# Kernel tuning notes

Hardware: AMD Instinct MI355X
Metric: run time of the kernel (lower is better)

## Reference

```python
import jax, jax.numpy as jnp
import numpy as np

POS_SCALE = 50.0
LEN_SCALE = 500.0

N_NODES = 100000
N_EDGES = 600000
IN_DIM = 128
HID_DIM = 128


def setup_inputs() -> dict:
    key = jax.random.key(0)
    ks = jax.random.split(key, 12)
    x = jax.random.normal(ks[0], (N_NODES, IN_DIM), dtype=jnp.float32)
    positions = jax.random.randint(ks[1], (N_NODES,), 0, 50, dtype=jnp.int64)
    lengths = jax.random.randint(ks[2], (N_NODES,), 0, 500, dtype=jnp.int64)
    edge_index = jax.random.randint(ks[3], (2, N_EDGES), 0, N_NODES, dtype=jnp.int64)
    reranker_scores = jax.random.normal(ks[4], (N_NODES,), dtype=jnp.float32)
    s = 1.0 / np.sqrt(IN_DIM + 2)
    fp_w = jax.random.uniform(ks[5], (IN_DIM + 2, IN_DIM), minval=-s, maxval=s, dtype=jnp.float32)
    fp_b = jnp.zeros((IN_DIM,), jnp.float32)
    s2 = 1.0 / np.sqrt(IN_DIM)
    lin_l_w = jax.random.uniform(ks[6], (IN_DIM, HID_DIM), minval=-s2, maxval=s2, dtype=jnp.float32)
    lin_l_b = jnp.zeros((HID_DIM,), jnp.float32)
    lin_r_w = jax.random.uniform(ks[7], (IN_DIM, HID_DIM), minval=-s2, maxval=s2, dtype=jnp.float32)
    res_w = jax.random.uniform(ks[8], (IN_DIM, HID_DIM), minval=-s2, maxval=s2, dtype=jnp.float32)
    res_b = jnp.zeros((HID_DIM,), jnp.float32)
    s3 = 1.0 / np.sqrt(HID_DIM)
    sh_w = jax.random.uniform(ks[9], (HID_DIM, 1), minval=-s3, maxval=s3, dtype=jnp.float32)
    sh_b = jnp.zeros((1,), jnp.float32)
    alpha = jnp.asarray(0.65, jnp.float32)
    return {
        "x": x, "positions": positions, "lengths": lengths,
        "edge_index": edge_index, "reranker_scores": reranker_scores,
        "fp_w": fp_w, "fp_b": fp_b,
        "lin_l_w": lin_l_w, "lin_l_b": lin_l_b, "lin_r_w": lin_r_w,
        "res_w": res_w, "res_b": res_b,
        "sh_w": sh_w, "sh_b": sh_b, "alpha": alpha,
    }


def reference(x, positions, lengths, edge_index, reranker_scores,
              fp_w, fp_b, lin_l_w, lin_l_b, lin_r_w, res_w, res_b,
              sh_w, sh_b, alpha):
    n = x.shape[0]
    # position/length features
    pos_feat = positions[:, None].astype(x.dtype) / POS_SCALE
    len_feat = lengths[:, None].astype(x.dtype) / LEN_SCALE
    xf = jnp.concatenate([x, pos_feat, len_feat], axis=-1)  # [N, D+2]
    xf = xf @ fp_w + fp_b                                   # [N, D]
    h_in = xf @ res_w + res_b                               # residual proj [N, H]
    # SAGEConv with mean aggregation: out = lin_l(mean_{j->i} x_j) + lin_r(x_i)
    src, dst = edge_index[0], edge_index[1]
    msg_sum = jax.ops.segment_sum(xf[src], dst, num_segments=n)          # [N, D]
    cnt = jax.ops.segment_sum(jnp.ones((src.shape[0], 1), xf.dtype), dst, num_segments=n)
    agg = msg_sum / jnp.maximum(cnt, 1.0)
    h = jax.nn.relu(agg @ lin_l_w + lin_l_b + xf @ lin_r_w)  # [N, H]
    # dropout is identity in eval mode
    h = h + h_in
    gnn_scores = (h @ sh_w + sh_b)[:, 0]                     # [N]
    a = jax.nn.sigmoid(alpha)
    return a * reranker_scores + (1.0 - a) * gnn_scores
```

## Files before the change

kernel.cpp:

```cpp
#include <hip/hip_runtime.h>
#include <hip/hip_bf16.h>
#include <cstdint>

#define D 128
#define LDSPITCH 136
#define CAP 32

typedef __attribute__((ext_vector_type(4))) float f32x4;
typedef __attribute__((ext_vector_type(8))) short s16x8;

__device__ __forceinline__ unsigned short f2b(float f) {
    union { float f; uint32_t u; } v; v.f = f;
    uint32_t b = v.u + 0x7fffu + ((v.u >> 16) & 1u);
    return (unsigned short)(b >> 16);
}
__device__ __forceinline__ float b2f(unsigned short u) {
    union { uint32_t u; float f; } v; v.u = ((uint32_t)u) << 16; return v.f;
}

__global__ __launch_bounds__(256) void k_prep(
    const float* __restrict__ fp_w, const float* __restrict__ lin_l_w,
    const float* __restrict__ lin_r_w,
    unsigned short* __restrict__ Btf, unsigned short* __restrict__ Btl,
    unsigned short* __restrict__ Btr,
    const float* __restrict__ res_w, const float* __restrict__ res_b,
    const float* __restrict__ sh_w, const float* __restrict__ sh_b,
    const float* __restrict__ alpha, float* __restrict__ c1, float* __restrict__ scal,
    int* __restrict__ cursor, int N) {
    int bid = blockIdx.x, tid = threadIdx.x;
    if (bid < 192) {
        int m = bid >> 6;
        int i = (bid & 63) * 256 + tid;
        const float* src = (m == 0) ? fp_w : (m == 1) ? lin_l_w : lin_r_w;
        unsigned short* dst = (m == 0) ? Btf : (m == 1) ? Btl : Btr;
        int k = i >> 7, n = i & 127;
        dst[n * D + k] = f2b(src[k * D + n]);
    } else if (bid == 192) {
        if (tid < 128) {
            float s = 0.f;
            for (int j = 0; j < D; ++j) s += res_w[tid * D + j] * sh_w[j];
            c1[tid] = s;
            if (tid == 0) {
                float c0 = 0.f;
                for (int j = 0; j < D; ++j) c0 += res_b[j] * sh_w[j];
                c0 += sh_b[0];
                float a = 1.f / (1.f + expf(-alpha[0]));
                scal[0] = a; scal[1] = c0;
            }
        }
    } else {
        int i = ((bid - 193) * 256 + tid) * 4;
        if (i < N) {
            if (i + 3 < N) *(int4*)(cursor + i) = (int4){0, 0, 0, 0};
            else { for (int k = i; k < N; ++k) cursor[k] = 0; }
        }
    }
}

__global__ __launch_bounds__(256) void k_gemm1(
    const float* __restrict__ x, unsigned short* __restrict__ xb,
    const int* __restrict__ positions, const int* __restrict__ lengths,
    const unsigned short* __restrict__ Btf,
    const float* __restrict__ fp_w, const float* __restrict__ fp_b,
    const float* __restrict__ c1, float* __restrict__ d1, int N, int mb,
    const int* __restrict__ ei, int* __restrict__ cursor, int* __restrict__ srcs, int E) {
    if (blockIdx.x >= mb) {
        int e = (blockIdx.x - mb) * 256 + threadIdx.x;
        if (e < E) {
            int src = ei[e];
            int dst = ei[E + e];
            int pos = atomicAdd(&cursor[dst], 1);
            if (pos < CAP) srcs[dst * CAP + pos] = src;
        }
        return;
    }
    int lane = threadIdx.x & 63;
    int wv = threadIdx.x >> 6;
    int col = lane & 15, q = lane >> 4;
    int row0 = blockIdx.x * 64 + wv * 16;
    int arow = row0 + col; if (arow > N - 1) arow = N - 1;

    f32x4 acc[8];
#pragma unroll
    for (int nt = 0; nt < 8; ++nt) acc[nt] = (f32x4){0.f, 0.f, 0.f, 0.f};

#pragma unroll
    for (int ks = 0; ks < 4; ++ks) {
        const float* xp = x + (size_t)arow * D + ks * 32 + q * 8;
        float4 a0 = *(const float4*)xp;
        float4 a1 = *(const float4*)(xp + 4);
        s16x8 af;
        af[0] = (short)f2b(a0.x); af[1] = (short)f2b(a0.y);
        af[2] = (short)f2b(a0.z); af[3] = (short)f2b(a0.w);
        af[4] = (short)f2b(a1.x); af[5] = (short)f2b(a1.y);
        af[6] = (short)f2b(a1.z); af[7] = (short)f2b(a1.w);
#pragma unroll
        for (int nt = 0; nt < 8; ++nt) {
            s16x8 bf = *(const s16x8*)(Btf + (size_t)(nt * 16 + col) * D + ks * 32 + q * 8);
            acc[nt] = __builtin_amdgcn_mfma_f32_16x16x32_bf16(af, bf, acc[nt], 0, 0, 0);
        }
    }

    float pf[4], lf[4];
#pragma unroll
    for (int r = 0; r < 4; ++r) {
        int rr = row0 + q * 4 + r; int rc = rr < N ? rr : N - 1;
        pf[r] = (float)positions[rc] * (1.0f / 50.0f);
        lf[r] = (float)lengths[rc] * (1.0f / 500.0f);
    }
    float sdot[4] = {0.f, 0.f, 0.f, 0.f};
#pragma unroll
    for (int nt = 0; nt < 8; ++nt) {
        int n = nt * 16 + col;
        float bias = fp_b[n];
        float w128 = fp_w[128 * D + n];
        float w129 = fp_w[129 * D + n];
        float c1v = c1[n];
#pragma unroll
        for (int r = 0; r < 4; ++r) {
            float t = acc[nt][r] + bias + pf[r] * w128 + lf[r] * w129;
            int rr = row0 + q * 4 + r;
            if (rr < N) xb[(size_t)rr * D + n] = f2b(t);
            sdot[r] += t * c1v;
        }
    }
#pragma unroll
    for (int r = 0; r < 4; ++r) {
        float s = sdot[r];
        s += __shfl_xor(s, 1, 64);
        s += __shfl_xor(s, 2, 64);
        s += __shfl_xor(s, 4, 64);
        s += __shfl_xor(s, 8, 64);
        if (col == 0) {
            int rr = row0 + q * 4 + r;
            if (rr < N) d1[rr] = s;
        }
    }
}

__global__ __launch_bounds__(256) void k_gemm2(
    const unsigned short* __restrict__ xfb,
    const int* __restrict__ cursor, const int* __restrict__ srcs,
    const unsigned short* __restrict__ Btl, const unsigned short* __restrict__ Btr,
    const float* __restrict__ lin_l_b, const float* __restrict__ sh_w,
    const float* __restrict__ rer, const float* __restrict__ d1,
    const float* __restrict__ scal, float* __restrict__ out, int N) {
    __shared__ unsigned short agg[64 * LDSPITCH];
    int lane = threadIdx.x & 63;
    int wv = threadIdx.x >> 6;
    int li = lane & 15, q = lane >> 4;
    int wrow0 = blockIdx.x * 64 + wv * 16;
    int Nm1 = N - 1;

    int rowc[4];
#pragma unroll
    for (int rr = 0; rr < 4; ++rr) {
        int row = wrow0 + rr * 4 + q;
        rowc[rr] = row < Nm1 ? row : Nm1;
    }
    int4 ia[4], ib[4];
    int deg[4];
#pragma unroll
    for (int rr = 0; rr < 4; ++rr) {
        const int* sp = srcs + (size_t)rowc[rr] * CAP;
        ia[rr] = *(const int4*)sp;
        ib[rr] = *(const int4*)(sp + 4);
        deg[rr] = cursor[rowc[rr]];
    }
    int arow = wrow0 + li; if (arow > Nm1) arow = Nm1;
    s16x8 afx[4];
#pragma unroll
    for (int ks = 0; ks < 4; ++ks)
        afx[ks] = *(const s16x8*)(xfb + (size_t)arow * D + ks * 32 + q * 8);

    float t[4][8];
#pragma unroll
    for (int rr = 0; rr < 4; ++rr)
#pragma unroll
        for (int k2 = 0; k2 < 8; ++k2) t[rr][k2] = 0.f;

#pragma unroll
    for (int rr = 0; rr < 4; ++rr) {
        int dg = deg[rr] > CAP ? CAP : deg[rr];
        int ix[8] = {ia[rr].x, ia[rr].y, ia[rr].z, ia[rr].w,
                     ib[rr].x, ib[rr].y, ib[rr].z, ib[rr].w};
        s16x8 v[8];
#pragma unroll
        for (int k = 0; k < 8; ++k) {
            int c = ix[k];
            c = c > 0 ? c : 0;
            c = c < Nm1 ? c : Nm1;
            v[k] = *(const s16x8*)(xfb + (size_t)c * D + li * 8);
        }
        float w[8];
#pragma unroll
        for (int k = 0; k < 8; ++k) w[k] = (k < dg) ? 1.f : 0.f;
#pragma unroll
        for (int k = 0; k < 8; ++k)
#pragma unroll
            for (int k2 = 0; k2 < 8; ++k2)
                t[rr][k2] += w[k] * b2f((unsigned short)v[k][k2]);
    }

#pragma unroll
    for (int rr = 0; rr < 4; ++rr) {
        int dg = deg[rr] > CAP ? CAP : deg[rr];
        if (dg > 8) {
            const int* sp = srcs + (size_t)rowc[rr] * CAP;
            for (int j = 8; j < dg; j += 8) {
                int4 ic = *(const int4*)(sp + j);
                int4 id = *(const int4*)(sp + j + 4);
                int ix[8] = {ic.x, ic.y, ic.z, ic.w, id.x, id.y, id.z, id.w};
                s16x8 v[8];
#pragma unroll
                for (int k = 0; k < 8; ++k) {
                    int c = ix[k];
                    c = c > 0 ? c : 0;
                    c = c < Nm1 ? c : Nm1;
                    v[k] = *(const s16x8*)(xfb + (size_t)c * D + li * 8);
                }
                float w[8];
#pragma unroll
                for (int k = 0; k < 8; ++k) w[k] = (j + k < dg) ? 1.f : 0.f;
#pragma unroll
                for (int k = 0; k < 8; ++k)
#pragma unroll
                    for (int k2 = 0; k2 < 8; ++k2)
                        t[rr][k2] += w[k] * b2f((unsigned short)v[k][k2]);
            }
        }
    }

#pragma unroll
    for (int rr = 0; rr < 4; ++rr) {
        int dg = deg[rr] > CAP ? CAP : deg[rr];
        float rc = 1.0f / (float)(dg > 0 ? dg : 1);
        s16x8 o;
#pragma unroll
        for (int k2 = 0; k2 < 8; ++k2) o[k2] = (short)f2b(t[rr][k2] * rc);
        *(s16x8*)(agg + (wv * 16 + rr * 4 + q) * LDSPITCH + li * 8) = o;
    }

    f32x4 acc[8];
#pragma unroll
    for (int nt = 0; nt < 8; ++nt) acc[nt] = (f32x4){0.f, 0.f, 0.f, 0.f};

#pragma unroll
    for (int ks = 0; ks < 4; ++ks) {
        s16x8 afa = *(const s16x8*)(agg + (wv * 16 + li) * LDSPITCH + ks * 32 + q * 8);
        s16x8 bfl[8];
#pragma unroll
        for (int nt = 0; nt < 8; ++nt)
            bfl[nt] = *(const s16x8*)(Btl + (size_t)(nt * 16 + li) * D + ks * 32 + q * 8);
#pragma unroll
        for (int nt = 0; nt < 8; ++nt)
            acc[nt] = __builtin_amdgcn_mfma_f32_16x16x32_bf16(afa, bfl[nt], acc[nt], 0, 0, 0);
        s16x8 bfr[8];
#pragma unroll
        for (int nt = 0; nt < 8; ++nt)
            bfr[nt] = *(const s16x8*)(Btr + (size_t)(nt * 16 + li) * D + ks * 32 + q * 8);
#pragma unroll
        for (int nt = 0; nt < 8; ++nt)
            acc[nt] = __builtin_amdgcn_mfma_f32_16x16x32_bf16(afx[ks], bfr[nt], acc[nt], 0, 0, 0);
    }

    float a = scal[0], c0 = scal[1];
    float sdot[4] = {0.f, 0.f, 0.f, 0.f};
#pragma unroll
    for (int nt = 0; nt < 8; ++nt) {
        int n = nt * 16 + li;
        float bias = lin_l_b[n];
        float shw = sh_w[n];
#pragma unroll
        for (int r = 0; r < 4; ++r) {
            float tt = acc[nt][r] + bias;
            sdot[r] += fmaxf(tt, 0.f) * shw;
        }
    }
#pragma unroll
    for (int r = 0; r < 4; ++r) {
        float s = sdot[r];
        s += __shfl_xor(s, 1, 64);
        s += __shfl_xor(s, 2, 64);
        s += __shfl_xor(s, 4, 64);
        s += __shfl_xor(s, 8, 64);
        if (li == 0) {
            int rr = wrow0 + q * 4 + r;
            if (rr < N) out[rr] = a * rer[rr] + (1.f - a) * (c0 + d1[rr] + s);
        }
    }
}

extern "C" void kernel_launch(void* const* d_in, const int* in_sizes, int n_in,
                              void* d_out, int out_size, void* d_ws, size_t ws_size,
                              hipStream_t stream) {
    const float* x        = (const float*)d_in[0];
    const int*   positions= (const int*)d_in[1];
    const int*   lengths  = (const int*)d_in[2];
    const int*   ei       = (const int*)d_in[3];
    const float* rer      = (const float*)d_in[4];
    const float* fp_w     = (const float*)d_in[5];
    const float* fp_b     = (const float*)d_in[6];
    const float* lin_l_w  = (const float*)d_in[7];
    const float* lin_l_b  = (const float*)d_in[8];
    const float* lin_r_w  = (const float*)d_in[9];
    const float* res_w    = (const float*)d_in[10];
    const float* res_b    = (const float*)d_in[11];
    const float* sh_w     = (const float*)d_in[12];
    const float* sh_b     = (const float*)d_in[13];
    const float* alpha    = (const float*)d_in[14];
    int N = in_sizes[1];
    int E = in_sizes[3] / 2;
    float* out = (float*)d_out;

    char* ws = (char*)d_ws;
    size_t off = 0;
    auto alloc = [&](size_t bytes) -> void* {
        void* p = ws + off;
        off = (off + bytes + 255) & ~(size_t)255;
        return p;
    };
    unsigned short* xb  = (unsigned short*)alloc((size_t)N * D * 2);
    int* srcs    = (int*)alloc((size_t)N * CAP * 4);
    int* cursor  = (int*)alloc((size_t)N * 4);
    float* d1    = (float*)alloc((size_t)N * 4);
    unsigned short* Btf = (unsigned short*)alloc(D * D * 2);
    unsigned short* Btl = (unsigned short*)alloc(D * D * 2);
    unsigned short* Btr = (unsigned short*)alloc(D * D * 2);
    float* c1    = (float*)alloc(D * 4);
    float* scal  = (float*)alloc(16);

    int mb = (N + 63) / 64;
    int cb = (E + 255) / 256;
    int zb = (N + 1023) / 1024;

    k_prep<<<193 + zb, 256, 0, stream>>>(fp_w, lin_l_w, lin_r_w, Btf, Btl, Btr,
                                         res_w, res_b, sh_w, sh_b, alpha, c1, scal,
                                         cursor, N);
    k_gemm1<<<mb + cb, 256, 0, stream>>>(x, xb, positions, lengths, Btf, fp_w, fp_b,
                                         c1, d1, N, mb, ei, cursor, srcs, E);
    k_gemm2<<<mb, 256, 0, stream>>>(xb, cursor, srcs, Btl, Btr, lin_l_b, sh_w, rer, d1, scal, out, N);
}
```

Baseline: 250.7 us.

## Replace per-node fixed-capacity adjacency with two-level bucketed CSR build

Edges are no longer scattered into a per-node padded slot array with one atomic per destination. They are first binned into coarse buckets of 256 destinations, and a new k_bucket kernel builds a compact CSR (row pointers plus sources) per bucket using LDS histograms and scans. The aggregation kernel then reads neighbor indices from the CSR. This cuts the padded 32-slot-per-node adjacency storage and the zeroing of the per-node cursor array, and removes the silent truncation at degree 32. In exchange it adds a kernel launch and an extra pass over the edges, and still silently drops edges past 2048 per bucket.

```diff
diff --git a/kernel.cpp b/kernel.cpp
--- a/kernel.cpp
+++ b/kernel.cpp
@@ -4,7 +4,7 @@
 
 #define D 128
 #define LDSPITCH 136
-#define CAP 32
+#define ECAP 2048
 
 typedef __attribute__((ext_vector_type(4))) float f32x4;
 typedef __attribute__((ext_vector_type(8))) short s16x8;
@@ -26,7 +26,7 @@
     const float* __restrict__ res_w, const float* __restrict__ res_b,
     const float* __restrict__ sh_w, const float* __restrict__ sh_b,
     const float* __restrict__ alpha, float* __restrict__ c1, float* __restrict__ scal,
-    int* __restrict__ cursor, int N) {
+    int* __restrict__ ccnt, int NB) {
     int bid = blockIdx.x, tid = threadIdx.x;
     if (bid < 192) {
         int m = bid >> 6;
@@ -35,7 +35,8 @@
         unsigned short* dst = (m == 0) ? Btf : (m == 1) ? Btl : Btr;
         int k = i >> 7, n = i & 127;
         dst[n * D + k] = f2b(src[k * D + n]);
-    } else if (bid == 192) {
+    } else {
+        for (int j = tid; j < NB; j += 256) ccnt[j] = 0;
         if (tid < 128) {
             float s = 0.f;
             for (int j = 0; j < D; ++j) s += res_w[tid * D + j] * sh_w[j];
@@ -48,12 +49,6 @@
                 scal[0] = a; scal[1] = c0;
             }
         }
-    } else {
-        int i = ((bid - 193) * 256 + tid) * 4;
-        if (i < N) {
-            if (i + 3 < N) *(int4*)(cursor + i) = (int4){0, 0, 0, 0};
-            else { for (int k = i; k < N; ++k) cursor[k] = 0; }
-        }
     }
 }
 
@@ -63,14 +58,15 @@
     const unsigned short* __restrict__ Btf,
     const float* __restrict__ fp_w, const float* __restrict__ fp_b,
     const float* __restrict__ c1, float* __restrict__ d1, int N, int mb,
-    const int* __restrict__ ei, int* __restrict__ cursor, int* __restrict__ srcs, int E) {
+    const int* __restrict__ ei, int* __restrict__ ccnt, int2* __restrict__ coarse, int E) {
     if (blockIdx.x >= mb) {
         int e = (blockIdx.x - mb) * 256 + threadIdx.x;
         if (e < E) {
             int src = ei[e];
             int dst = ei[E + e];
-            int pos = atomicAdd(&cursor[dst], 1);
-            if (pos < CAP) srcs[dst * CAP + pos] = src;
+            int b = dst >> 8;
+            int pos = atomicAdd(&ccnt[b], 1);
+            if (pos < ECAP) coarse[(size_t)b * ECAP + pos] = make_int2(src, dst);
         }
         return;
     }
@@ -138,9 +134,58 @@
     }
 }
 
+__global__ __launch_bounds__(256) void k_bucket(
+    const int2* __restrict__ coarse, const int* __restrict__ ccnt,
+    int* __restrict__ csr, int* __restrict__ rp, int NB, int N) {
+    __shared__ int2 pb[ECAP];
+    __shared__ int hist[256];
+    __shared__ int epfx[256];
+    __shared__ int slot[256];
+    __shared__ int red[256];
+    int tid = threadIdx.x, b = blockIdx.x;
+    int cnt = ccnt[b]; if (cnt > ECAP) cnt = ECAP;
+
+    for (int i = tid; i < cnt; i += 256) pb[i] = coarse[(size_t)b * ECAP + i];
+    hist[tid] = 0;
+    int part = 0;
+    for (int j = tid; j < b; j += 256) { int c = ccnt[j]; part += c > ECAP ? ECAP : c; }
+    red[tid] = part;
+    __syncthreads();
+
+    for (int i = tid; i < cnt; i += 256) atomicAdd(&hist[pb[i].y & 255], 1);
+    for (int off = 128; off; off >>= 1) {
+        if (tid < off) red[tid] += red[tid + off];
+        __syncthreads();
+    }
+    int gb = red[0];
+    int h0 = hist[tid];
+    epfx[tid] = h0;
+    __syncthreads();
+    for (int off = 1; off < 256; off <<= 1) {
+        int u = (tid >= off) ? epfx[tid - off] : 0;
+        __syncthreads();
+        if (tid >= off) epfx[tid] += u;
+        __syncthreads();
+    }
+    int excl = epfx[tid] - h0;
+    int g = b * 256 + tid;
+    if (g < N) rp[g] = gb + excl;
+    if (b == NB - 1 && tid == 255) rp[N] = gb + epfx[255];
+
+    slot[tid] = 0;
+    __syncthreads();
+    epfx[tid] = excl;
+    __syncthreads();
+    for (int i = tid; i < cnt; i += 256) {
+        int l = pb[i].y & 255;
+        int p = atomicAdd(&slot[l], 1);
+        csr[gb + epfx[l] + p] = pb[i].x;
+    }
+}
+
 __global__ __launch_bounds__(256) void k_gemm2(
     const unsigned short* __restrict__ xfb,
-    const int* __restrict__ cursor, const int* __restrict__ srcs,
+    const int* __restrict__ rp, const int* __restrict__ csr,
     const unsigned short* __restrict__ Btl, const unsigned short* __restrict__ Btr,
     const float* __restrict__ lin_l_b, const float* __restrict__ sh_w,
     const float* __restrict__ rer, const float* __restrict__ d1,
@@ -158,20 +203,23 @@
         int row = wrow0 + rr * 4 + q;
         rowc[rr] = row < Nm1 ? row : Nm1;
     }
-    int4 ia[4], ib[4];
-    int deg[4];
-#pragma unroll
-    for (int rr = 0; rr < 4; ++rr) {
-        const int* sp = srcs + (size_t)rowc[rr] * CAP;
-        ia[rr] = *(const int4*)sp;
-        ib[rr] = *(const int4*)(sp + 4);
-        deg[rr] = cursor[rowc[rr]];
+    int bse[4], dgq[4];
+#pragma unroll
+    for (int rr = 0; rr < 4; ++rr) {
+        bse[rr] = rp[rowc[rr]];
+        dgq[rr] = rp[rowc[rr] + 1] - bse[rr];
     }
     int arow = wrow0 + li; if (arow > Nm1) arow = Nm1;
     s16x8 afx[4];
 #pragma unroll
     for (int ks = 0; ks < 4; ++ks)
         afx[ks] = *(const s16x8*)(xfb + (size_t)arow * D + ks * 32 + q * 8);
+    int ix[4][8];
+#pragma unroll
+    for (int rr = 0; rr < 4; ++rr)
+#pragma unroll
+        for (int k = 0; k < 8; ++k)
+            ix[rr][k] = csr[bse[rr] + k];
 
     float t[4][8];
 #pragma unroll
@@ -181,13 +229,11 @@
 
 #pragma unroll
     for (int rr = 0; rr < 4; ++rr) {
-        int dg = deg[rr] > CAP ? CAP : deg[rr];
-        int ix[8] = {ia[rr].x, ia[rr].y, ia[rr].z, ia[rr].w,
-                     ib[rr].x, ib[rr].y, ib[rr].z, ib[rr].w};
+        int dg = dgq[rr];
         s16x8 v[8];
 #pragma unroll
         for (int k = 0; k < 8; ++k) {
-            int c = ix[k];
+            int c = ix[rr][k];
             c = c > 0 ? c : 0;
             c = c < Nm1 ? c : Nm1;
             v[k] = *(const s16x8*)(xfb + (size_t)c * D + li * 8);
@@ -204,17 +250,16 @@
 
 #pragma unroll
     for (int rr = 0; rr < 4; ++rr) {
-        int dg = deg[rr] > CAP ? CAP : deg[rr];
+        int dg = dgq[rr];
         if (dg > 8) {
-            const int* sp = srcs + (size_t)rowc[rr] * CAP;
             for (int j = 8; j < dg; j += 8) {
-                int4 ic = *(const int4*)(sp + j);
-                int4 id = *(const int4*)(sp + j + 4);
-                int ix[8] = {ic.x, ic.y, ic.z, ic.w, id.x, id.y, id.z, id.w};
+                int jx[8];
+#pragma unroll
+                for (int k = 0; k < 8; ++k) jx[k] = csr[bse[rr] + j + k];
                 s16x8 v[8];
 #pragma unroll
                 for (int k = 0; k < 8; ++k) {
-                    int c = ix[k];
+                    int c = jx[k];
                     c = c > 0 ? c : 0;
                     c = c < Nm1 ? c : Nm1;
                     v[k] = *(const s16x8*)(xfb + (size_t)c * D + li * 8);
@@ -233,7 +278,7 @@
 
 #pragma unroll
     for (int rr = 0; rr < 4; ++rr) {
-        int dg = deg[rr] > CAP ? CAP : deg[rr];
+        int dg = dgq[rr];
         float rc = 1.0f / (float)(dg > 0 ? dg : 1);
         s16x8 o;
 #pragma unroll
@@ -313,6 +358,8 @@
     int E = in_sizes[3] / 2;
     float* out = (float*)d_out;
 
+    int NB = (N + 255) >> 8;
+
     char* ws = (char*)d_ws;
     size_t off = 0;
     auto alloc = [&](size_t bytes) -> void* {
@@ -321,8 +368,10 @@
         return p;
     };
     unsigned short* xb  = (unsigned short*)alloc((size_t)N * D * 2);
-    int* srcs    = (int*)alloc((size_t)N * CAP * 4);
-    int* cursor  = (int*)alloc((size_t)N * 4);
+    int2* coarse = (int2*)alloc((size_t)NB * ECAP * 8);
+    int* ccnt    = (int*)alloc((size_t)NB * 4);
+    int* csr     = (int*)alloc(((size_t)E + 64) * 4);
+    int* rp      = (int*)alloc(((size_t)N + 1) * 4);
     float* d1    = (float*)alloc((size_t)N * 4);
     unsigned short* Btf = (unsigned short*)alloc(D * D * 2);
     unsigned short* Btl = (unsigned short*)alloc(D * D * 2);
@@ -332,12 +381,12 @@
 
     int mb = (N + 63) / 64;
     int cb = (E + 255) / 256;
-    int zb = (N + 1023) / 1024;
-
-    k_prep<<<193 + zb, 256, 0, stream>>>(fp_w, lin_l_w, lin_r_w, Btf, Btl, Btr,
-                                         res_w, res_b, sh_w, sh_b, alpha, c1, scal,
-                                         cursor, N);
+
+    k_prep<<<193, 256, 0, stream>>>(fp_w, lin_l_w, lin_r_w, Btf, Btl, Btr,
+                                    res_w, res_b, sh_w, sh_b, alpha, c1, scal,
+                                    ccnt, NB);
     k_gemm1<<<mb + cb, 256, 0, stream>>>(x, xb, positions, lengths, Btf, fp_w, fp_b,
-                                         c1, d1, N, mb, ei, cursor, srcs, E);
-    k_gemm2<<<mb, 256, 0, stream>>>(xb, cursor, srcs, Btl, Btr, lin_l_b, sh_w, rer, d1, scal, out, N);
-}
+                                         c1, d1, N, mb, ei, ccnt, coarse, E);
+    k_bucket<<<NB, 256, 0, stream>>>(coarse, ccnt, csr, rp, NB, N);
+    k_gemm2<<<mb, 256, 0, stream>>>(xb, rp, csr, Btl, Btr, lin_l_b, sh_w, rer, d1, scal, out, N);
+}
```

Result: slower. 433.9 us (+73.1%).

## Replace per-node atomic adjacency with bucketed counting sort by destination block

Applied to the files above, without the earlier changes.

The per-node global-atomic adjacency build (fixed CAP slots per node) is replaced by a two-level counting sort. Edges are first histogrammed into 64-node destination buckets in LDS, the buckets are prefix-scanned, and then edges are scattered into a compact coarse array. k_gemm2 loads its block's bucket into an LDS dense adjacency with shared-memory atomics before gathering. This aims to remove contended global atomics, the scattered writes into a large N*CAP array, and the cursor zeroing. In exchange it adds two small scan kernels, one of them a single-block serial scan, plus extra launches. It also packs the node index into 17 bits, which assumes N is at most 131072.

```diff
diff --git a/kernel.cpp b/kernel.cpp
--- a/kernel.cpp
+++ b/kernel.cpp
@@ -4,7 +4,10 @@
 
 #define D 128
 #define LDSPITCH 136
-#define CAP 32
+#define LB 64
+#define DCAP 32
+#define NBLK 64
+#define NBMAX 2048
 
 typedef __attribute__((ext_vector_type(4))) float f32x4;
 typedef __attribute__((ext_vector_type(8))) short s16x8;
@@ -26,7 +29,8 @@
     const float* __restrict__ res_w, const float* __restrict__ res_b,
     const float* __restrict__ sh_w, const float* __restrict__ sh_b,
     const float* __restrict__ alpha, float* __restrict__ c1, float* __restrict__ scal,
-    int* __restrict__ cursor, int N) {
+    const int* __restrict__ ei, int* __restrict__ histg, int E, int EBLK, int NB) {
+    __shared__ int h[NBMAX];
     int bid = blockIdx.x, tid = threadIdx.x;
     if (bid < 192) {
         int m = bid >> 6;
@@ -49,12 +53,51 @@
             }
         }
     } else {
-        int i = ((bid - 193) * 256 + tid) * 4;
-        if (i < N) {
-            if (i + 3 < N) *(int4*)(cursor + i) = (int4){0, 0, 0, 0};
-            else { for (int k = i; k < N; ++k) cursor[k] = 0; }
-        }
-    }
+        int k = bid - 193;
+        for (int j = tid; j < NB; j += 256) h[j] = 0;
+        __syncthreads();
+        int s = k * EBLK, e = s + EBLK; if (e > E) e = E;
+        for (int i = s + tid; i < e; i += 256)
+            atomicAdd(&h[ei[E + i] >> 6], 1);
+        __syncthreads();
+        for (int j = tid; j < NB; j += 256) histg[j * NBLK + k] = h[j];
+    }
+}
+
+__global__ __launch_bounds__(256) void k_scan1(
+    int* __restrict__ histg, int* __restrict__ total, int NB) {
+    int b = blockIdx.x * 256 + threadIdx.x;
+    if (b >= NB) return;
+    int* p = histg + (size_t)b * NBLK;
+    int run = 0;
+#pragma unroll 8
+    for (int k = 0; k < NBLK; ++k) { int t = p[k]; p[k] = run; run += t; }
+    total[b] = run;
+}
+
+__global__ __launch_bounds__(256) void k_scan2(
+    const int* __restrict__ total, int* __restrict__ base, int NB) {
+    __shared__ int sh[256];
+    int tid = threadIdx.x;
+    int carry = 0;
+    int nch = (NB + 255) >> 8;
+    for (int c = 0; c < nch; ++c) {
+        int idx = c * 256 + tid;
+        int v = idx < NB ? total[idx] : 0;
+        sh[tid] = v;
+        __syncthreads();
+        for (int off = 1; off < 256; off <<= 1) {
+            int u = (tid >= off) ? sh[tid - off] : 0;
+            __syncthreads();
+            if (tid >= off) sh[tid] += u;
+            __syncthreads();
+        }
+        if (idx < NB) base[idx] = carry + sh[tid] - v;
+        int chtot = sh[255];
+        __syncthreads();
+        carry += chtot;
+    }
+    if (tid == 0) base[NB] = carry;
 }
 
 __global__ __launch_bounds__(256) void k_gemm1(
@@ -63,14 +106,21 @@
     const unsigned short* __restrict__ Btf,
     const float* __restrict__ fp_w, const float* __restrict__ fp_b,
     const float* __restrict__ c1, float* __restrict__ d1, int N, int mb,
-    const int* __restrict__ ei, int* __restrict__ cursor, int* __restrict__ srcs, int E) {
+    const int* __restrict__ ei, const int* __restrict__ histg,
+    const int* __restrict__ base, int* __restrict__ coarse, int E, int EBLK, int NB) {
+    __shared__ int cur[NBMAX];
     if (blockIdx.x >= mb) {
-        int e = (blockIdx.x - mb) * 256 + threadIdx.x;
-        if (e < E) {
-            int src = ei[e];
-            int dst = ei[E + e];
-            int pos = atomicAdd(&cursor[dst], 1);
-            if (pos < CAP) srcs[dst * CAP + pos] = src;
+        int tid = threadIdx.x;
+        int k = blockIdx.x - mb;
+        for (int j = tid; j < NB; j += 256)
+            cur[j] = base[j] + histg[(size_t)j * NBLK + k];
+        __syncthreads();
+        int s = k * EBLK, e = s + EBLK; if (e > E) e = E;
+        for (int i = s + tid; i < e; i += 256) {
+            int sv = ei[i];
+            int d  = ei[E + i];
+            int p = atomicAdd(&cur[d >> 6], 1);
+            coarse[p] = sv | ((d & 63) << 17);
         }
         return;
     }
@@ -140,50 +190,58 @@
 
 __global__ __launch_bounds__(256) void k_gemm2(
     const unsigned short* __restrict__ xfb,
-    const int* __restrict__ cursor, const int* __restrict__ srcs,
+    const int* __restrict__ base, const int* __restrict__ coarse,
     const unsigned short* __restrict__ Btl, const unsigned short* __restrict__ Btr,
     const float* __restrict__ lin_l_b, const float* __restrict__ sh_w,
     const float* __restrict__ rer, const float* __restrict__ d1,
     const float* __restrict__ scal, float* __restrict__ out, int N) {
     __shared__ unsigned short agg[64 * LDSPITCH];
-    int lane = threadIdx.x & 63;
-    int wv = threadIdx.x >> 6;
+    __shared__ int dense[64][DCAP];
+    __shared__ int cnt64[64];
+    int tid = threadIdx.x;
+    int lane = tid & 63;
+    int wv = tid >> 6;
     int li = lane & 15, q = lane >> 4;
     int wrow0 = blockIdx.x * 64 + wv * 16;
     int Nm1 = N - 1;
 
-    int rowc[4];
-#pragma unroll
-    for (int rr = 0; rr < 4; ++rr) {
-        int row = wrow0 + rr * 4 + q;
-        rowc[rr] = row < Nm1 ? row : Nm1;
-    }
-    int4 ia[4], ib[4];
-    int deg[4];
-#pragma unroll
-    for (int rr = 0; rr < 4; ++rr) {
-        const int* sp = srcs + (size_t)rowc[rr] * CAP;
-        ia[rr] = *(const int4*)sp;
-        ib[rr] = *(const int4*)(sp + 4);
-        deg[rr] = cursor[rowc[rr]];
-    }
     int arow = wrow0 + li; if (arow > Nm1) arow = Nm1;
     s16x8 afx[4];
 #pragma unroll
     for (int ks = 0; ks < 4; ++ks)
         afx[ks] = *(const s16x8*)(xfb + (size_t)arow * D + ks * 32 + q * 8);
 
+    int b0 = base[blockIdx.x], cnt = base[blockIdx.x + 1] - b0;
+    if (tid < 64) cnt64[tid] = 0;
+    __syncthreads();
+    for (int i = tid; i < cnt; i += 256) {
+        int v = coarse[b0 + i];
+        int l = v >> 17;
+        int p = atomicAdd(&cnt64[l], 1);
+        if (p < DCAP) dense[l][p] = v & 0x1ffff;
+    }
+    __syncthreads();
+
     float t[4][8];
 #pragma unroll
     for (int rr = 0; rr < 4; ++rr)
 #pragma unroll
         for (int k2 = 0; k2 < 8; ++k2) t[rr][k2] = 0.f;
 
+    int dgq[4];
 #pragma unroll
     for (int rr = 0; rr < 4; ++rr) {
-        int dg = deg[rr] > CAP ? CAP : deg[rr];
-        int ix[8] = {ia[rr].x, ia[rr].y, ia[rr].z, ia[rr].w,
-                     ib[rr].x, ib[rr].y, ib[rr].z, ib[rr].w};
+        int dg = cnt64[wv * 16 + rr * 4 + q];
+        dgq[rr] = dg > DCAP ? DCAP : dg;
+    }
+
+#pragma unroll
+    for (int rr = 0; rr < 4; ++rr) {
+        int dg = dgq[rr];
+        const int* dr = &dense[wv * 16 + rr * 4 + q][0];
+        int4 ja = *(const int4*)dr;
+        int4 jb = *(const int4*)(dr + 4);
+        int ix[8] = {ja.x, ja.y, ja.z, ja.w, jb.x, jb.y, jb.z, jb.w};
         s16x8 v[8];
 #pragma unroll
         for (int k = 0; k < 8; ++k) {
@@ -204,13 +262,13 @@
 
 #pragma unroll
     for (int rr = 0; rr < 4; ++rr) {
-        int dg = deg[rr] > CAP ? CAP : deg[rr];
+        int dg = dgq[rr];
         if (dg > 8) {
-            const int* sp = srcs + (size_t)rowc[rr] * CAP;
+            const int* dr = &dense[wv * 16 + rr * 4 + q][0];
             for (int j = 8; j < dg; j += 8) {
-                int4 ic = *(const int4*)(sp + j);
-                int4 id = *(const int4*)(sp + j + 4);
-                int ix[8] = {ic.x, ic.y, ic.z, ic.w, id.x, id.y, id.z, id.w};
+                int4 jc = *(const int4*)(dr + j);
+                int4 jd = *(const int4*)(dr + j + 4);
+                int ix[8] = {jc.x, jc.y, jc.z, jc.w, jd.x, jd.y, jd.z, jd.w};
                 s16x8 v[8];
 #pragma unroll
                 for (int k = 0; k < 8; ++k) {
@@ -233,7 +291,7 @@
 
 #pragma unroll
     for (int rr = 0; rr < 4; ++rr) {
-        int dg = deg[rr] > CAP ? CAP : deg[rr];
+        int dg = dgq[rr];
         float rc = 1.0f / (float)(dg > 0 ? dg : 1);
         s16x8 o;
 #pragma unroll
@@ -313,6 +371,10 @@
     int E = in_sizes[3] / 2;
     float* out = (float*)d_out;
 
+    int NB = (N + LB - 1) / LB;
+    int EBLK = (E + NBLK - 1) / NBLK;
+    int mb = (N + 63) / 64;
+
     char* ws = (char*)d_ws;
     size_t off = 0;
     auto alloc = [&](size_t bytes) -> void* {
@@ -321,8 +383,10 @@
         return p;
     };
     unsigned short* xb  = (unsigned short*)alloc((size_t)N * D * 2);
-    int* srcs    = (int*)alloc((size_t)N * CAP * 4);
-    int* cursor  = (int*)alloc((size_t)N * 4);
+    int* coarse  = (int*)alloc(((size_t)E + 64) * 4);
+    int* histg   = (int*)alloc((size_t)NB * NBLK * 4);
+    int* total   = (int*)alloc((size_t)NB * 4);
+    int* base    = (int*)alloc(((size_t)NB + 1) * 4);
     float* d1    = (float*)alloc((size_t)N * 4);
     unsigned short* Btf = (unsigned short*)alloc(D * D * 2);
     unsigned short* Btl = (unsigned short*)alloc(D * D * 2);
@@ -330,14 +394,14 @@
     float* c1    = (float*)alloc(D * 4);
     float* scal  = (float*)alloc(16);
 
-    int mb = (N + 63) / 64;
-    int cb = (E + 255) / 256;
-    int zb = (N + 1023) / 1024;
-
-    k_prep<<<193 + zb, 256, 0, stream>>>(fp_w, lin_l_w, lin_r_w, Btf, Btl, Btr,
-                                         res_w, res_b, sh_w, sh_b, alpha, c1, scal,
-                                         cursor, N);
-    k_gemm1<<<mb + cb, 256, 0, stream>>>(x, xb, positions, lengths, Btf, fp_w, fp_b,
-                                         c1, d1, N, mb, ei, cursor, srcs, E);
-    k_gemm2<<<mb, 256, 0, stream>>>(xb, cursor, srcs, Btl, Btr, lin_l_b, sh_w, rer, d1, scal, out, N);
-}
+    k_prep<<<193 + NBLK, 256, 0, stream>>>(fp_w, lin_l_w, lin_r_w, Btf, Btl, Btr,
+                                           res_w, res_b, sh_w, sh_b, alpha, c1, scal,
+                                           ei, histg, E, EBLK, NB);
+    k_scan1<<<(NB + 255) / 256, 256, 0, stream>>>(histg, total, NB);
+    k_scan2<<<1, 256, 0, stream>>>(total, base, NB);
+    k_gemm1<<<mb + NBLK, 256, 0, stream>>>(x, xb, positions, lengths, Btf, fp_w, fp_b,
+                                           c1, d1, N, mb, ei, histg, base, coarse,
+                                           E, EBLK, NB);
+    k_gemm2<<<mb, 256, 0, stream>>>(xb, base, coarse, Btl, Btr, lin_l_b, sh_w,
+                                    rer, d1, scal, out, N);
+}
```

Result: slower. 261.0 us (+4.1%).
